# Kernel tuning notes

Measured on AMD Instinct MI355X. Metric: run time of the kernel, lower is better.

The kernel has to match this reference:

```python
import jax, jax.numpy as jnp
import numpy as np

B, S, D, H = 2, 2048, 1024, 16
DH = D // H  # 64


def _rotate_half(t):
    x1, x2 = jnp.split(t, 2, axis=-1)
    return jnp.concatenate([-x2, x1], axis=-1)


def setup_inputs() -> dict:
    key = jax.random.key(0)
    ks = jax.random.split(key, 11)
    x = jax.random.normal(ks[0], (B, S, D), dtype=jnp.float32)
    mask = jax.random.randint(ks[1], (B, S), 0, 2, dtype=jnp.int32)
    scale = 0.02
    wq = jax.random.normal(ks[2], (D, D), dtype=jnp.float32) * scale
    bq = jnp.zeros((D,), dtype=jnp.float32)
    wk = jax.random.normal(ks[3], (D, D), dtype=jnp.float32) * scale
    bk = jnp.zeros((D,), dtype=jnp.float32)
    wv = jax.random.normal(ks[4], (D, D), dtype=jnp.float32) * scale
    bv = jnp.zeros((D,), dtype=jnp.float32)
    wo = jax.random.normal(ks[5], (D, D), dtype=jnp.float32) * scale
    bo = jnp.zeros((D,), dtype=jnp.float32)
    return {"x": x, "mask": mask, "wq": wq, "bq": bq, "wk": wk, "bk": bk,
            "wv": wv, "bv": bv, "wo": wo, "bo": bo}


def reference(x, mask, wq, bq, wk, bk, wv, bv, wo, bo):
    b, s, d = x.shape
    # QKV projections, split heads -> [B, H, S, DH]
    q = (x @ wq + bq).reshape(b, s, H, DH).transpose(0, 2, 1, 3)
    k = (x @ wk + bk).reshape(b, s, H, DH).transpose(0, 2, 1, 3)
    v = (x @ wv + bv).reshape(b, s, H, DH).transpose(0, 2, 1, 3)
    # RoPE exactly as in source: repeat(cos,2) paired with half-split rotate
    pos = jnp.arange(s, dtype=jnp.float32)
    inv_freq = 1.0 / (10000.0 ** (jnp.arange(0, DH, 2, dtype=jnp.float32) / DH))
    angle = pos[:, None] * inv_freq[None, :]            # [S, DH/2]
    cos = jnp.repeat(jnp.cos(angle), 2, axis=-1)[None, None]  # [1,1,S,DH]
    sin = jnp.repeat(jnp.sin(angle), 2, axis=-1)[None, None]
    q = q * cos + _rotate_half(q) * sin
    k = k * cos + _rotate_half(k) * sin
    # scaled dot-product attention with additive mask
    logits = jnp.einsum('bhqd,bhkd->bhqk', q, k) / jnp.sqrt(jnp.float32(DH))
    m = mask.astype(jnp.float32)[:, None, None, :]      # [B,1,1,S]
    logits = logits + m * (-1e9)
    attn = jax.nn.softmax(logits, axis=-1)
    out = jnp.einsum('bhqk,bhkd->bhqd', attn, v)
    out = out.transpose(0, 2, 1, 3).reshape(b, s, d)
    return out @ wo + bo
```

## Files before the change

### kernel.cpp

```cpp
#include <hip/hip_runtime.h>
#include <math.h>

#define BB 2
#define SS 2048
#define DD 1024
#define HH 16

typedef unsigned short u16;
using bf16x8 = __attribute__((ext_vector_type(8))) short;
using f32x4  = __attribute__((ext_vector_type(4))) float;

#define LOG2E 1.44269504f


__device__ __forceinline__ u16 f2bf(float f) {
    unsigned u = __float_as_uint(f);
    unsigned r = u + 0x7fffu + ((u >> 16) & 1u);
    return (u16)(r >> 16);
}

__device__ __forceinline__ void gload_lds16(const void* g, const void* l) {
    __builtin_amdgcn_global_load_lds(
        (const __attribute__((address_space(1))) unsigned int*)(unsigned long long)g,
        (__attribute__((address_space(3))) unsigned int*)(unsigned int)(unsigned long long)l,
        16, 0, 0);
}

__global__ void prep_tw(const float* __restrict__ x, u16* __restrict__ xb,
                        float* __restrict__ cost, float* __restrict__ sint,
                        const int* __restrict__ mask, float* __restrict__ mb,
                        const float* __restrict__ w0, const float* __restrict__ w1,
                        const float* __restrict__ w2, const float* __restrict__ w3,
                        u16* __restrict__ o0, u16* __restrict__ o1,
                        u16* __restrict__ o2, u16* __restrict__ o3) {
    __shared__ float tb[32][33];
    int bid = blockIdx.x;
    int t   = threadIdx.x;
    if (bid < 4096) {
        int gid = bid * 256 + t;
        {
            int i = gid * 4;
            float4 v = *(const float4*)(x + i);
            ushort4 o;
            o.x = f2bf(v.x); o.y = f2bf(v.y); o.z = f2bf(v.z); o.w = f2bf(v.w);
            *(ushort4*)(xb + i) = o;
        }
        if (bid < 256) {
            int j   = gid >> 11;
            int pos = gid & 2047;
            double inv = pow(10000.0, -(double)j / 32.0);
            double ang = (double)pos * inv;
            cost[gid] = (float)cos(ang);
            sint[gid] = (float)sin(ang);
        }
        if (bid >= 256 && bid < 272) {
            int i = gid - 65536;
            mb[i] = -1.44269504e9f * (float)mask[i];
        }
    } else {
        int tid = bid - 4096;
        int z   = tid >> 10;
        int rem = tid & 1023;
        int bxt = rem & 31;
        int byt = rem >> 5;
        const float* in = (z == 0) ? w0 : (z == 1) ? w1 : (z == 2) ? w2 : w3;
        u16* out        = (z == 0) ? o0 : (z == 1) ? o1 : (z == 2) ? o2 : o3;
        int tx = t & 31, ty = t >> 5;
        int n = bxt * 32 + tx;
        for (int i = ty; i < 32; i += 8)
            tb[i][tx] = in[(size_t)(byt * 32 + i) * 1024 + n];
        __syncthreads();
        int k = byt * 32 + tx;
        for (int i = ty; i < 32; i += 8)
            out[(size_t)(bxt * 32 + i) * 1024 + k] = f2bf(tb[tx][i]);
    }
}

__global__ __launch_bounds__(256)
void qkv_gemm(const u16* __restrict__ xb,
              const u16* __restrict__ wtq, const u16* __restrict__ wtk, const u16* __restrict__ wtv,
              const float* __restrict__ bq, const float* __restrict__ bk, const float* __restrict__ bv,
              const float* __restrict__ cost, const float* __restrict__ sint,
              u16* __restrict__ qo, u16* __restrict__ ko, u16* __restrict__ vo)
{
    __shared__ u16 Al[128 * 32];
    __shared__ u16 Bl[128 * 32];

    int bx = blockIdx.x;
    int which = bx >> 3;
    int n0 = (bx & 7) << 7;
    int m0 = blockIdx.y << 7;
    const u16*  wt    = (which == 0) ? wtq : (which == 1) ? wtk : wtv;
    const float* bias = (which == 0) ? bq  : (which == 1) ? bk  : bv;

    int t = threadIdx.x;
    int wid = t >> 6, lane = t & 63;
    int wr = wid >> 1, wc = wid & 1;
    int fr = lane & 15, fq = lane >> 4;

    f32x4 acc[4][4];
    #pragma unroll
    for (int m = 0; m < 4; ++m)
        #pragma unroll
        for (int n = 0; n < 4; ++n)
            #pragma unroll
            for (int r = 0; r < 4; ++r) acc[m][n][r] = 0.f;

    int srow = (lane >> 2);
    int skof = (lane & 3) << 3;

    for (int k0 = 0; k0 < 1024; k0 += 32) {
        __syncthreads();
        #pragma unroll
        for (int c = 0; c < 2; ++c) {
            int chunk = wid * 2 + c;
            int row = (chunk << 4) + srow;
            gload_lds16(xb + (size_t)(m0 + row) * 1024 + k0 + skof, &Al[chunk << 9]);
            gload_lds16(wt + (size_t)(n0 + row) * 1024 + k0 + skof, &Bl[chunk << 9]);
        }
        __syncthreads();

        bf16x8 af[4], bf[4];
        #pragma unroll
        for (int m = 0; m < 4; ++m)
            af[m] = *(const bf16x8*)&Al[((wr << 6) + (m << 4) + fr) * 32 + (fq << 3)];
        #pragma unroll
        for (int n = 0; n < 4; ++n)
            bf[n] = *(const bf16x8*)&Bl[((wc << 6) + (n << 4) + fr) * 32 + (fq << 3)];
        #pragma unroll
        for (int m = 0; m < 4; ++m)
            #pragma unroll
            for (int n = 0; n < 4; ++n)
                acc[m][n] = __builtin_amdgcn_mfma_f32_16x16x32_bf16(af[m], bf[n], acc[m][n], 0, 0, 0);
    }

    if (which < 2) {
        u16* outp = (which == 0) ? qo : ko;
        const float qs = (which == 0) ? 0.125f * LOG2E : 1.0f;
        #pragma unroll
        for (int n = 0; n < 2; ++n) {
            int col = n0 + (wc << 6) + (n << 4) + fr;
            int h = col >> 6;
            int d = col & 63;
            float b1 = bias[col], b2 = bias[col + 32];
            int a1 = d >> 1;
            #pragma unroll
            for (int mm = 0; mm < 4; ++mm) {
                int mi0 = m0 + (wr << 6) + (mm << 4) + (fq << 2);
                int bi = mi0 >> 11, s0 = mi0 & 2047;
                float4 c1 = *(const float4*)(cost + (a1 << 11) + s0);
                float4 s1 = *(const float4*)(sint + (a1 << 11) + s0);
                float4 c2 = *(const float4*)(cost + ((a1 + 16) << 11) + s0);
                float4 s2 = *(const float4*)(sint + ((a1 + 16) << 11) + s0);
                const float* c1p = (const float*)&c1;
                const float* s1p = (const float*)&s1;
                const float* c2p = (const float*)&c2;
                const float* s2p = (const float*)&s2;
                #pragma unroll
                for (int j = 0; j < 4; ++j) {
                    float x1 = acc[mm][n][j]     + b1;
                    float x2 = acc[mm][n + 2][j] + b2;
                    size_t base = ((size_t)(bi * HH + h) * SS + s0 + j) << 6;
                    outp[base + d]      = f2bf((x1 * c1p[j] - x2 * s1p[j]) * qs);
                    outp[base + d + 32] = f2bf((x2 * c2p[j] + x1 * s2p[j]) * qs);
                }
            }
        }
    } else {
        #pragma unroll
        for (int n = 0; n < 4; ++n) {
            int col = n0 + (wc << 6) + (n << 4) + fr;
            int h = col >> 6, d = col & 63;
            float bb = bias[col];
            #pragma unroll
            for (int mm = 0; mm < 4; ++mm) {
                #pragma unroll
                for (int j = 0; j < 4; ++j) {
                    int mi = m0 + (wr << 6) + (mm << 4) + (fq << 2) + j;
                    int bi = mi >> 11, s = mi & 2047;
                    vo[((((size_t)(bi * HH + h)) << 6) + d) * SS + s] = f2bf(acc[mm][n][j] + bb);
                }
            }
        }
    }
}

__global__ __launch_bounds__(256, 4)
void attn(const u16* __restrict__ qb, const u16* __restrict__ kb, const u16* __restrict__ vt,
          const float* __restrict__ mbias, u16* __restrict__ preb)
{
    __shared__ u16 Kl[2][4096];
    __shared__ u16 Vl[2][4096];
    __shared__ u16 Pl[4][1024];

    const int bid = blockIdx.x;
    const int xcd = bid & 7;
    const int idx = bid >> 3;
    const int bh  = (xcd << 2) | (idx >> 5);
    const int qb0 = (idx & 31) << 6;
    const int b   = bh >> 4;
    const int t   = threadIdx.x;
    const int w   = t >> 6;
    const int lane = t & 63;
    const int fr  = lane & 15;
    const int fq  = lane >> 4;
    const int swz = (fr & 7) << 4;

    const char* kbase = (const char*)(kb + ((size_t)bh << 17));
    const char* vbase = (const char*)(vt + ((size_t)bh << 17));
    const float* mbp  = mbias + (b << 11);

    const int sbo = ((t & 7) << 4) ^ (((t >> 3) & 7) << 4);

    const int qrow = qb0 + (w << 4) + fr;
    const u16* qp = qb + (((size_t)bh << 11) + qrow) * 64 + (fq << 3);
    bf16x8 qf0 = *(const bf16x8*)qp;
    bf16x8 qf1 = *(const bf16x8*)(qp + 32);

    f32x4 o[4];
    #pragma unroll
    for (int n = 0; n < 4; ++n)
        #pragma unroll
        for (int r = 0; r < 4; ++r) o[n][r] = 0.f;
    float mrun = -INFINITY, lrun = 0.f;

    auto STAGE = [&](int buf, int kt) {
        #pragma unroll
        for (int c = 0; c < 2; ++c) {
            int row = (c << 5) + (t >> 3);
            gload_lds16(kbase + ((size_t)(kt << 6) + row) * 128 + sbo,
                        (const char*)&Kl[buf][0] + (c << 12) + t * 16);
            gload_lds16(vbase + (size_t)row * 4096 + (kt << 7) + sbo,
                        (const char*)&Vl[buf][0] + (c << 12) + t * 16);
        }
    };

    STAGE(0, 0);
    __syncthreads();

    for (int kt = 0; kt < 32; ++kt) {
        const int cur = kt & 1;

        if (kt < 31) STAGE(cur ^ 1, kt + 1);

        f32x4 sv[4];
        #pragma unroll
        for (int g = 0; g < 4; ++g)
            #pragma unroll
            for (int r = 0; r < 4; ++r) sv[g][r] = 0.f;

        const char* Kb = (const char*)&Kl[cur][0];
        __builtin_amdgcn_s_setprio(1);
        #pragma unroll
        for (int g = 0; g < 4; ++g) {
            int row = (g << 4) + fr;
            bf16x8 kf0 = *(const bf16x8*)(Kb + row * 128 + ((fq << 4) ^ swz));
            bf16x8 kf1 = *(const bf16x8*)(Kb + row * 128 + (((fq << 4) + 64) ^ swz));
            sv[g] = __builtin_amdgcn_mfma_f32_16x16x32_bf16(kf0, qf0, sv[g], 0, 0, 0);
            sv[g] = __builtin_amdgcn_mfma_f32_16x16x32_bf16(kf1, qf1, sv[g], 0, 0, 0);
        }
        __builtin_amdgcn_s_setprio(0);

        float tm = -INFINITY;
        #pragma unroll
        for (int g = 0; g < 4; ++g) {
            const float4 m4 = *(const float4*)(mbp + (kt << 6) + (g << 4) + (fq << 2));
            sv[g][0] += m4.x; sv[g][1] += m4.y; sv[g][2] += m4.z; sv[g][3] += m4.w;
            tm = fmaxf(tm, fmaxf(fmaxf(sv[g][0], sv[g][1]), fmaxf(sv[g][2], sv[g][3])));
        }
        tm = fmaxf(tm, __shfl_xor(tm, 16));
        tm = fmaxf(tm, __shfl_xor(tm, 32));

        if (!__all(tm <= mrun + 11.0f)) {
            float newm = fmaxf(mrun, tm);
            float scale = __builtin_amdgcn_exp2f(mrun - newm);
            lrun *= scale;
            #pragma unroll
            for (int j = 0; j < 4; ++j) {
                float sj = __shfl(scale, (lane & 48) + (fq << 2) + j);
                #pragma unroll
                for (int n = 0; n < 4; ++n) o[n][j] *= sj;
            }
            mrun = newm;
        }

        float ps = 0.f;
        #pragma unroll
        for (int g = 0; g < 4; ++g) {
            float p0 = __builtin_amdgcn_exp2f(sv[g][0] - mrun);
            float p1 = __builtin_amdgcn_exp2f(sv[g][1] - mrun);
            float p2 = __builtin_amdgcn_exp2f(sv[g][2] - mrun);
            float p3 = __builtin_amdgcn_exp2f(sv[g][3] - mrun);
            ps += (p0 + p1) + (p2 + p3);
            unsigned r0, r1;
            asm("v_cvt_pk_bf16_f32 %0, %1, %2" : "=v"(r0) : "v"(p0), "v"(p1));
            asm("v_cvt_pk_bf16_f32 %0, %1, %2" : "=v"(r1) : "v"(p2), "v"(p3));
            uint2 pw; pw.x = r0; pw.y = r1;
            *(uint2*)((char*)&Pl[w][0] + fr * 128 + (((g << 5) + (fq << 3)) ^ swz)) = pw;
        }
        ps += __shfl_xor(ps, 16);
        ps += __shfl_xor(ps, 32);
        lrun += ps;

        __builtin_amdgcn_s_setprio(1);
        #pragma unroll
        for (int kk = 0; kk < 2; ++kk) {
            bf16x8 pa = *(const bf16x8*)((const char*)&Pl[w][0] + fr * 128 + (((fq << 4) + (kk << 6)) ^ swz));
            #pragma unroll
            for (int n = 0; n < 4; ++n) {
                int row = (n << 4) + fr;
                bf16x8 vf = *(const bf16x8*)((const char*)&Vl[cur][0] + row * 128 + (((fq << 4) + (kk << 6)) ^ swz));
                o[n] = __builtin_amdgcn_mfma_f32_16x16x32_bf16(pa, vf, o[n], 0, 0, 0);
            }
        }
        __builtin_amdgcn_s_setprio(0);
        __syncthreads();
    }

    #pragma unroll
    for (int j = 0; j < 4; ++j) {
        float lj = __shfl(lrun, (lane & 48) + (fq << 2) + j);
        float inv = 1.0f / lj;
        int qr = qb0 + (w << 4) + (fq << 2) + j;
        u16* op = preb + ((size_t)((b << 11) + qr) << 10) + ((bh & 15) << 6) + fr;
        #pragma unroll
        for (int n = 0; n < 4; ++n)
            op[n << 4] = f2bf(o[n][j] * inv);
    }
}

__global__ __launch_bounds__(256)
void out_gemm(const u16* __restrict__ pre, const u16* __restrict__ wto,
              const float* __restrict__ bo, float* __restrict__ outp)
{
    __shared__ u16 Al[128 * 32];
    __shared__ u16 Bl[128 * 32];

    int n0 = blockIdx.x << 7;
    int m0 = blockIdx.y << 7;

    int t = threadIdx.x;
    int wid = t >> 6, lane = t & 63;
    int wr = wid >> 1, wc = wid & 1;
    int fr = lane & 15, fq = lane >> 4;

    f32x4 acc[4][4];
    #pragma unroll
    for (int m = 0; m < 4; ++m)
        #pragma unroll
        for (int n = 0; n < 4; ++n)
            #pragma unroll
            for (int r = 0; r < 4; ++r) acc[m][n][r] = 0.f;

    int srow = (lane >> 2);
    int skof = (lane & 3) << 3;

    for (int k0 = 0; k0 < 1024; k0 += 32) {
        __syncthreads();
        #pragma unroll
        for (int c = 0; c < 2; ++c) {
            int chunk = wid * 2 + c;
            int row = (chunk << 4) + srow;
            gload_lds16(pre + (size_t)(m0 + row) * 1024 + k0 + skof, &Al[chunk << 9]);
            gload_lds16(wto + (size_t)(n0 + row) * 1024 + k0 + skof, &Bl[chunk << 9]);
        }
        __syncthreads();

        bf16x8 af[4], bf[4];
        #pragma unroll
        for (int m = 0; m < 4; ++m)
            af[m] = *(const bf16x8*)&Al[((wr << 6) + (m << 4) + fr) * 32 + (fq << 3)];
        #pragma unroll
        for (int n = 0; n < 4; ++n)
            bf[n] = *(const bf16x8*)&Bl[((wc << 6) + (n << 4) + fr) * 32 + (fq << 3)];
        #pragma unroll
        for (int m = 0; m < 4; ++m)
            #pragma unroll
            for (int n = 0; n < 4; ++n)
                acc[m][n] = __builtin_amdgcn_mfma_f32_16x16x32_bf16(af[m], bf[n], acc[m][n], 0, 0, 0);
    }

    #pragma unroll
    for (int n = 0; n < 4; ++n) {
        int col = n0 + (wc << 6) + (n << 4) + fr;
        float bb = bo[col];
        #pragma unroll
        for (int m = 0; m < 4; ++m) {
            #pragma unroll
            for (int j = 0; j < 4; ++j) {
                int mi = m0 + (wr << 6) + (m << 4) + (fq << 2) + j;
                outp[(size_t)mi * 1024 + col] = acc[m][n][j] + bb;
            }
        }
    }
}

extern "C" void kernel_launch(void* const* d_in, const int* in_sizes, int n_in,
                              void* d_out, int out_size, void* d_ws, size_t ws_size,
                              hipStream_t stream) {
    const float* x    = (const float*)d_in[0];
    const int*   mask = (const int*)  d_in[1];
    const float* wq   = (const float*)d_in[2];
    const float* bq   = (const float*)d_in[3];
    const float* wk   = (const float*)d_in[4];
    const float* bk   = (const float*)d_in[5];
    const float* wv   = (const float*)d_in[6];
    const float* bv   = (const float*)d_in[7];
    const float* wo   = (const float*)d_in[8];
    const float* bo   = (const float*)d_in[9];
    float* out = (float*)d_out;
    float* ws  = (float*)d_ws;

    float* cosT  = ws;
    float* sinT  = ws + 65536;
    float* mbias = ws + 131072;
    u16* xb    = (u16*)(ws + 135168);
    u16* wtq   = xb    + 4194304;
    u16* wtk   = wtq   + 1048576;
    u16* wtv   = wtk   + 1048576;
    u16* wto   = wtv   + 1048576;
    u16* qbuf  = wto   + 1048576;
    u16* kbuf  = qbuf  + 4194304;
    u16* vtbuf = kbuf  + 4194304;
    u16* preb  = vtbuf + 4194304;

    hipLaunchKernelGGL(prep_tw, dim3(8192), dim3(256), 0, stream,
                       x, xb, cosT, sinT, mask, mbias,
                       wq, wk, wv, wo, wtq, wtk, wtv, wto);
    hipLaunchKernelGGL(qkv_gemm, dim3(24, 32), dim3(256), 0, stream,
                       xb, wtq, wtk, wtv, bq, bk, bv, cosT, sinT, qbuf, kbuf, vtbuf);
    hipLaunchKernelGGL(attn, dim3(1024), dim3(256), 0, stream,
                       qbuf, kbuf, vtbuf, mbias, preb);
    hipLaunchKernelGGL(out_gemm, dim3(8, 32), dim3(256), 0, stream, preb, wto, bo, out);
}
```

Measured before the change: 227.5 us.

## Rewrite QKV GEMM as 256x256-tile 8-wave ping-pong pipelined kernel

Replaces the 128x128 single-buffered QKV GEMM with a 512-thread, 256x256-tile kernel. It uses a double-buffered, XOR-swizzled 128KB LDS and interleaves async global-to-LDS loads with MFMA phases under explicit barriers and priority hints. Workgroups are remapped across XCDs, and the V-transpose stores become 4-wide vector stores. The aim is to hide load latency and raise MFMA utilisation, at the cost of one block per CU and only 192 workgroups, which may underfill the GPU.

Measured after the change: 217.1 us. 1.05x faster.

```diff
diff --git a/kernel.cpp b/kernel.cpp
--- a/kernel.cpp
+++ b/kernel.cpp
@@ -76,78 +76,161 @@
     }
 }
 
-__global__ __launch_bounds__(256)
-void qkv_gemm(const u16* __restrict__ xb,
-              const u16* __restrict__ wtq, const u16* __restrict__ wtk, const u16* __restrict__ wtv,
-              const float* __restrict__ bq, const float* __restrict__ bk, const float* __restrict__ bv,
-              const float* __restrict__ cost, const float* __restrict__ sint,
-              u16* __restrict__ qo, u16* __restrict__ ko, u16* __restrict__ vo)
+__global__ __launch_bounds__(512, 1)
+void qkv_gemm8(const u16* __restrict__ xb,
+               const u16* __restrict__ wtq, const u16* __restrict__ wtk, const u16* __restrict__ wtv,
+               const float* __restrict__ bq, const float* __restrict__ bk, const float* __restrict__ bv,
+               const float* __restrict__ cost, const float* __restrict__ sint,
+               u16* __restrict__ qo, u16* __restrict__ ko, u16* __restrict__ vo)
 {
-    __shared__ u16 Al[128 * 32];
-    __shared__ u16 Bl[128 * 32];
-
-    int bx = blockIdx.x;
-    int which = bx >> 3;
-    int n0 = (bx & 7) << 7;
-    int m0 = blockIdx.y << 7;
+    __shared__ u16 L[65536];
+
+    const int bid  = blockIdx.x;
+    const int wgid = (bid & 7) * 24 + (bid >> 3);
+    const int mt = wgid / 12, nt = wgid % 12;
+    const int which = nt >> 2;
+    const int m0  = mt << 8;
+    const int nw0 = (nt & 3) << 8;
+
     const u16*  wt    = (which == 0) ? wtq : (which == 1) ? wtk : wtv;
     const float* bias = (which == 0) ? bq  : (which == 1) ? bk  : bv;
 
-    int t = threadIdx.x;
-    int wid = t >> 6, lane = t & 63;
-    int wr = wid >> 1, wc = wid & 1;
-    int fr = lane & 15, fq = lane >> 4;
-
-    f32x4 acc[4][4];
+    const int t    = threadIdx.x;
+    const int wid  = t >> 6, lane = t & 63;
+    const int wm   = wid >> 2, wn = wid & 3;
+    const int fr   = lane & 15, fq = lane >> 4;
+
+    const int sr = t >> 3;
+    const int sc = ((t & 7) ^ (sr & 7)) << 3;
+
+    auto STAGE = [&](int buf, int kt, int kind) {
+        int sk = (kt & 15) << 6;
+        const u16* src = (kind < 2)
+            ? xb + (size_t)(m0  + ((kind & 1) << 7)) * 1024 + sk
+            : wt + (size_t)(nw0 + ((kind & 1) << 7)) * 1024 + sk;
+        char* dst = (char*)L + (buf << 16) + (kind << 14) + t * 16;
+        gload_lds16(src + (size_t)sr * 1024 + sc, dst);
+        gload_lds16(src + (size_t)(64 + sr) * 1024 + sc, dst + 8192);
+    };
+
+    bf16x8 af[4][2];
+    bf16x8 bf0[2][2], bf1[2][2];
+    f32x4  acc[8][4];
     #pragma unroll
-    for (int m = 0; m < 4; ++m)
+    for (int i = 0; i < 8; ++i)
         #pragma unroll
         for (int n = 0; n < 4; ++n)
             #pragma unroll
-            for (int r = 0; r < 4; ++r) acc[m][n][r] = 0.f;
-
-    int srow = (lane >> 2);
-    int skof = (lane & 3) << 3;
-
-    for (int k0 = 0; k0 < 1024; k0 += 32) {
-        __syncthreads();
-        #pragma unroll
-        for (int c = 0; c < 2; ++c) {
-            int chunk = wid * 2 + c;
-            int row = (chunk << 4) + srow;
-            gload_lds16(xb + (size_t)(m0 + row) * 1024 + k0 + skof, &Al[chunk << 9]);
-            gload_lds16(wt + (size_t)(n0 + row) * 1024 + k0 + skof, &Bl[chunk << 9]);
-        }
-        __syncthreads();
-
-        bf16x8 af[4], bf[4];
-        #pragma unroll
-        for (int m = 0; m < 4; ++m)
-            af[m] = *(const bf16x8*)&Al[((wr << 6) + (m << 4) + fr) * 32 + (fq << 3)];
-        #pragma unroll
-        for (int n = 0; n < 4; ++n)
-            bf[n] = *(const bf16x8*)&Bl[((wc << 6) + (n << 4) + fr) * 32 + (fq << 3)];
-        #pragma unroll
-        for (int m = 0; m < 4; ++m)
-            #pragma unroll
-            for (int n = 0; n < 4; ++n)
-                acc[m][n] = __builtin_amdgcn_mfma_f32_16x16x32_bf16(af[m], bf[n], acc[m][n], 0, 0, 0);
-    }
-
+            for (int r = 0; r < 4; ++r) acc[i][n][r] = 0.f;
+
+    auto LDA = [&](int mg, int buf) {
+        #pragma unroll
+        for (int i = 0; i < 4; ++i) {
+            int lr = (i << 5) + (wm << 4) + fr;
+            const char* rb = (const char*)L + (buf << 16) + (mg << 14) + lr * 128;
+            #pragma unroll
+            for (int kk = 0; kk < 2; ++kk)
+                af[i][kk] = *(const bf16x8*)(rb + ((((kk << 2) + fq) ^ (lr & 7)) << 4));
+        }
+    };
+    auto LDB = [&](bf16x8 (&bf)[2][2], int ng, int buf) {
+        #pragma unroll
+        for (int n = 0; n < 2; ++n) {
+            int lr = ((wn & 1) << 6) + (((ng << 1) + n) << 4) + fr;
+            const char* rb = (const char*)L + (buf << 16) + ((2 + (wn >> 1)) << 14) + lr * 128;
+            #pragma unroll
+            for (int kk = 0; kk < 2; ++kk)
+                bf[n][kk] = *(const bf16x8*)(rb + ((((kk << 2) + fq) ^ (lr & 7)) << 4));
+        }
+    };
+    auto MM = [&](bf16x8 (&bf)[2][2], int mg, int ng) {
+        __builtin_amdgcn_s_setprio(1);
+        #pragma unroll
+        for (int kk = 0; kk < 2; ++kk)
+            #pragma unroll
+            for (int i = 0; i < 4; ++i)
+                #pragma unroll
+                for (int n = 0; n < 2; ++n)
+                    acc[(mg << 2) + i][(ng << 1) + n] =
+                        __builtin_amdgcn_mfma_f32_16x16x32_bf16(
+                            af[i][kk], bf[n][kk], acc[(mg << 2) + i][(ng << 1) + n], 0, 0, 0);
+        __builtin_amdgcn_s_setprio(0);
+    };
+
+    STAGE(0, 0, 0); STAGE(0, 0, 1); STAGE(0, 0, 2); STAGE(0, 0, 3);
+    STAGE(1, 1, 0); STAGE(1, 1, 2); STAGE(1, 1, 3);
+    asm volatile("s_waitcnt vmcnt(6)" ::: "memory");
+    __builtin_amdgcn_s_barrier();
+    __builtin_amdgcn_sched_barrier(0);
+
+    #pragma unroll 1
+    for (int it = 0; it < 8; ++it) {
+        const int e2 = 2 * it + 2, o2 = 2 * it + 3;
+        LDA(0, 0); LDB(bf0, 0, 0);
+        __builtin_amdgcn_sched_barrier(0);
+        STAGE(1, 2 * it + 1, 1);
+        __builtin_amdgcn_s_barrier();
+        MM(bf0, 0, 0);
+        __builtin_amdgcn_s_barrier();
+        LDB(bf1, 1, 0);
+        __builtin_amdgcn_sched_barrier(0);
+        STAGE(0, e2, 0);
+        __builtin_amdgcn_s_barrier();
+        MM(bf1, 0, 1);
+        __builtin_amdgcn_s_barrier();
+        LDA(1, 0);
+        __builtin_amdgcn_sched_barrier(0);
+        STAGE(0, e2, 2);
+        __builtin_amdgcn_s_barrier();
+        MM(bf0, 1, 0);
+        __builtin_amdgcn_s_barrier();
+        STAGE(0, e2, 3);
+        asm volatile("s_waitcnt vmcnt(6)" ::: "memory");
+        __builtin_amdgcn_s_barrier();
+        __builtin_amdgcn_sched_barrier(0);
+        MM(bf1, 1, 1);
+        __builtin_amdgcn_s_barrier();
+        LDA(0, 1); LDB(bf0, 0, 1);
+        __builtin_amdgcn_sched_barrier(0);
+        STAGE(0, e2, 1);
+        __builtin_amdgcn_s_barrier();
+        MM(bf0, 0, 0);
+        __builtin_amdgcn_s_barrier();
+        LDB(bf1, 1, 1);
+        __builtin_amdgcn_sched_barrier(0);
+        STAGE(1, o2, 0);
+        __builtin_amdgcn_s_barrier();
+        MM(bf1, 0, 1);
+        __builtin_amdgcn_s_barrier();
+        LDA(1, 1);
+        __builtin_amdgcn_sched_barrier(0);
+        STAGE(1, o2, 2);
+        __builtin_amdgcn_s_barrier();
+        MM(bf0, 1, 0);
+        __builtin_amdgcn_s_barrier();
+        STAGE(1, o2, 3);
+        asm volatile("s_waitcnt vmcnt(6)" ::: "memory");
+        __builtin_amdgcn_s_barrier();
+        __builtin_amdgcn_sched_barrier(0);
+        MM(bf1, 1, 1);
+        __builtin_amdgcn_s_barrier();
+    }
+    asm volatile("s_waitcnt vmcnt(0)" ::: "memory");
+
+    const int h = ((nt & 3) << 2) + wn;
     if (which < 2) {
         u16* outp = (which == 0) ? qo : ko;
         const float qs = (which == 0) ? 0.125f * LOG2E : 1.0f;
         #pragma unroll
-        for (int n = 0; n < 2; ++n) {
-            int col = n0 + (wc << 6) + (n << 4) + fr;
-            int h = col >> 6;
-            int d = col & 63;
-            float b1 = bias[col], b2 = bias[col + 32];
+        for (int ni = 0; ni < 2; ++ni) {
+            int d    = (ni << 4) + fr;
+            int colw = nw0 + (wn << 6) + d;
+            float b1 = bias[colw], b2 = bias[colw + 32];
             int a1 = d >> 1;
             #pragma unroll
-            for (int mm = 0; mm < 4; ++mm) {
-                int mi0 = m0 + (wr << 6) + (mm << 4) + (fq << 2);
-                int bi = mi0 >> 11, s0 = mi0 & 2047;
+            for (int mi = 0; mi < 8; ++mi) {
+                int row = m0 + (mi << 5) + (wm << 4) + (fq << 2);
+                int bi = row >> 11, s0 = row & 2047;
                 float4 c1 = *(const float4*)(cost + (a1 << 11) + s0);
                 float4 s1 = *(const float4*)(sint + (a1 << 11) + s0);
                 float4 c2 = *(const float4*)(cost + ((a1 + 16) << 11) + s0);
@@ -158,8 +241,8 @@
                 const float* s2p = (const float*)&s2;
                 #pragma unroll
                 for (int j = 0; j < 4; ++j) {
-                    float x1 = acc[mm][n][j]     + b1;
-                    float x2 = acc[mm][n + 2][j] + b2;
+                    float x1 = acc[mi][ni][j]     + b1;
+                    float x2 = acc[mi][ni + 2][j] + b2;
                     size_t base = ((size_t)(bi * HH + h) * SS + s0 + j) << 6;
                     outp[base + d]      = f2bf((x1 * c1p[j] - x2 * s1p[j]) * qs);
                     outp[base + d + 32] = f2bf((x2 * c2p[j] + x1 * s2p[j]) * qs);
@@ -168,18 +251,19 @@
         }
     } else {
         #pragma unroll
-        for (int n = 0; n < 4; ++n) {
-            int col = n0 + (wc << 6) + (n << 4) + fr;
-            int h = col >> 6, d = col & 63;
-            float bb = bias[col];
-            #pragma unroll
-            for (int mm = 0; mm < 4; ++mm) {
-                #pragma unroll
-                for (int j = 0; j < 4; ++j) {
-                    int mi = m0 + (wr << 6) + (mm << 4) + (fq << 2) + j;
-                    int bi = mi >> 11, s = mi & 2047;
-                    vo[((((size_t)(bi * HH + h)) << 6) + d) * SS + s] = f2bf(acc[mm][n][j] + bb);
-                }
+        for (int ni = 0; ni < 4; ++ni) {
+            int d = (ni << 4) + fr;
+            float bb = bias[nw0 + (wn << 6) + d];
+            #pragma unroll
+            for (int mi = 0; mi < 8; ++mi) {
+                int row = m0 + (mi << 5) + (wm << 4) + (fq << 2);
+                int bi = row >> 11, s0 = row & 2047;
+                ushort4 pv;
+                pv.x = f2bf(acc[mi][ni][0] + bb);
+                pv.y = f2bf(acc[mi][ni][1] + bb);
+                pv.z = f2bf(acc[mi][ni][2] + bb);
+                pv.w = f2bf(acc[mi][ni][3] + bb);
+                *(ushort4*)(vo + ((size_t)(((bi * HH + h) << 6) + d)) * SS + s0) = pv;
             }
         }
     }
@@ -427,7 +511,7 @@
     hipLaunchKernelGGL(prep_tw, dim3(8192), dim3(256), 0, stream,
                        x, xb, cosT, sinT, mask, mbias,
                        wq, wk, wv, wo, wtq, wtk, wtv, wto);
-    hipLaunchKernelGGL(qkv_gemm, dim3(24, 32), dim3(256), 0, stream,
+    hipLaunchKernelGGL(qkv_gemm8, dim3(192), dim3(512), 0, stream,
                        xb, wtq, wtk, wtv, bq, bk, bv, cosT, sinT, qbuf, kbuf, vtbuf);
     hipLaunchKernelGGL(attn, dim3(1024), dim3(256), 0, stream,
                        qbuf, kbuf, vtbuf, mbias, preb);
```
